# Optimization experiments

Measured on AMD Instinct MI355X. Metric: run time of the kernel, lower is better.

The kernel has to match this reference:

```python
import jax, jax.numpy as jnp
import numpy as np

B, N, K_NB, C, KERNEL, OUT = 32, 128, 16, 1024, 8, 1024
TWO_PI = 2.0 * np.pi
EPS = 1e-14


def setup_inputs() -> dict:
    key = jax.random.key(0)
    ks = jax.random.split(key, 9)
    return {
        "node_feats": jax.random.normal(ks[0], (B, N, C), dtype=jnp.float32),
        "node_centre": jax.random.uniform(ks[1], (B, N, 2), dtype=jnp.float32),
        "neighbor_idx": jax.random.randint(ks[2], (B, N, K_NB), 0, N, dtype=jnp.int32),
        "graph_weights": jax.random.uniform(ks[3], (B, N, K_NB), dtype=jnp.float32),
        "mean_rho": jax.random.uniform(ks[4], (1, KERNEL), dtype=jnp.float32),
        "mean_theta": jax.random.uniform(ks[5], (1, KERNEL), minval=-np.pi, maxval=np.pi, dtype=jnp.float32),
        "precision_rho": jax.random.uniform(ks[6], (1, KERNEL), dtype=jnp.float32),
        "precision_theta": jax.random.uniform(ks[7], (1, KERNEL), dtype=jnp.float32),
        "conv_w": jax.random.normal(ks[8], (KERNEL, C, OUT // KERNEL), dtype=jnp.float32) * 0.02,
    }


def _gaussian_weights(node_centre, neighbor_idx, mean_rho, mean_theta, precision_rho, precision_theta):
    # gather neighbor centres per batch: [B,N,K,2]
    centre_j = jax.vmap(lambda c, idx: c[idx])(node_centre, neighbor_idx)
    diff = node_centre[:, :, None, :] - centre_j           # node_i - node_j
    cx, cy = diff[..., 0], diff[..., 1]                    # chunk order: x first
    rho = jnp.sqrt(cx ** 2 + cy ** 2)                      # [B,N,K]
    theta = jnp.arctan2(cx, cy)                            # note: atan2(x, y) as in source
    d_rho = (rho[..., None] - mean_rho[0]) ** 2            # [B,N,K,KERNEL]
    w_rho = jnp.exp(-0.5 * d_rho / (EPS + precision_rho[0] ** 2))
    a1 = jnp.abs(theta[..., None] - mean_theta[0])
    a2 = jnp.abs(TWO_PI - a1)
    w_theta = jnp.exp(-0.5 * jnp.minimum(a1, a2) ** 2 / (EPS + precision_theta[0] ** 2))
    w = w_rho * w_theta
    w = jnp.where(jnp.isnan(w), 0.0, w)
    return w / jnp.sum(w, axis=-1, keepdims=True)          # normalize over kernel dim


def reference(node_feats, node_centre, neighbor_idx, graph_weights,
              mean_rho, mean_theta, precision_rho, precision_theta, conv_w):
    gw = _gaussian_weights(node_centre, neighbor_idx, mean_rho, mean_theta,
                           precision_rho, precision_theta)       # [B,N,K,KERNEL]
    edge_w = graph_weights[..., None] * gw                        # use_graph_weights=True
    # gather neighbor features per batch: [B,N,K,C]
    feats_j = jax.vmap(lambda f, idx: f[idx])(node_feats, neighbor_idx)
    # bmm aggregation: [B,N,KERNEL,C]
    agg = jnp.einsum('bnkm,bnkc->bnmc', edge_w, feats_j)
    # per-kernel linear (no bias) then concat: [B,N,KERNEL,OUT//KERNEL] -> [B,N,OUT]
    out = jnp.einsum('bnmc,mcd->bnmd', agg, conv_w)
    out = out.reshape(node_feats.shape[0], node_feats.shape[1], -1)
    return jax.nn.relu(out)
```

## Files before the change

### kernel.cpp

```cpp
#include <hip/hip_runtime.h>
#include <hip/hip_bf16.h>

#define B_   32
#define N_   128
#define KNB  16
#define C_   1024
#define KER  8
#define DOUT 128
#define OUTC 1024

typedef __attribute__((ext_vector_type(8))) short bf16x8;
typedef __attribute__((ext_vector_type(4))) float f32x4;

__device__ __forceinline__ ushort f2bf(float f) {
    unsigned u = __builtin_bit_cast(unsigned, f);
    unsigned r = (u + 0x7FFFu + ((u >> 16) & 1u)) >> 16;
    return (ushort)r;
}


__global__ __launch_bounds__(256) void k_prep(const float* __restrict__ F,
                                              ushort* __restrict__ Fpack,
                                              const float* __restrict__ W,
                                              ushort* __restrict__ Wpack,
                                              const float* __restrict__ centre,
                                              const int* __restrict__ nidx,
                                              const float* __restrict__ gw,
                                              const float* __restrict__ mr,
                                              const float* __restrict__ mt,
                                              const float* __restrict__ pr,
                                              const float* __restrict__ pt,
                                              float* __restrict__ ew) {
    __shared__ ushort Pt[16 * 1032];
    int bid = blockIdx.x;
    int t   = threadIdx.x;

    if (bid < 256) {
        int R0 = bid * 16;
#pragma unroll
        for (int it = 0; it < 16; ++it) {
            float4 v = *(const float4*)(F + (size_t)(R0 + it) * C_ + t * 4);
            ushort* d = Pt + it * 1032 + t * 4;
            d[0] = f2bf(v.x); d[1] = f2bf(v.y); d[2] = f2bf(v.z); d[3] = f2bf(v.w);
        }
        __syncthreads();
        ushort* dst = Fpack + (size_t)bid * 16384;
#pragma unroll
        for (int it = 0; it < 8; ++it) {
            int c  = it * 256 + t;
            int ln = c & 63, s = (c >> 6) & 15, kq = c >> 10;
            int lr = ln & 15, kg = ln >> 4;
            bf16x8 v = *(const bf16x8*)(Pt + lr * 1032 + kq * 512 + s * 32 + kg * 8);
            *(bf16x8*)(dst + (size_t)c * 8) = v;
        }
    } else if (bid < 320) {
        int b2 = bid - 256;
        int m  = b2 >> 3;
        int D0 = ((b2 >> 2) & 1) * 64 + (b2 & 3) * 16;
#pragma unroll
        for (int it = 0; it < 16; ++it) {
            int f  = it * 256 + t;
            int c  = f >> 2, q4 = f & 3;
            float4 v = *(const float4*)(W + (size_t)m * (C_ * DOUT) + (size_t)c * DOUT + D0 + q4 * 4);
            Pt[(q4 * 4 + 0) * 1032 + c] = f2bf(v.x);
            Pt[(q4 * 4 + 1) * 1032 + c] = f2bf(v.y);
            Pt[(q4 * 4 + 2) * 1032 + c] = f2bf(v.z);
            Pt[(q4 * 4 + 3) * 1032 + c] = f2bf(v.w);
        }
        __syncthreads();
        ushort* dst = Wpack + (size_t)b2 * 16384;
#pragma unroll
        for (int it = 0; it < 8; ++it) {
            int c  = it * 256 + t;
            int ln = c & 63, s = (c >> 6) & 15, kq = c >> 10;
            int lr = ln & 15, kg = ln >> 4;
            bf16x8 v = *(const bf16x8*)(Pt + lr * 1032 + kq * 512 + s * 32 + kg * 8);
            *(bf16x8*)(dst + (size_t)c * 8) = v;
        }
    } else {
        int tt = (bid - 320) * 256 + t;
        int bn = tt >> 4;
        int b  = bn >> 7;
        float2 ci = *(const float2*)(centre + (size_t)bn * 2);
        int j = nidx[tt];
        float2 cj = *(const float2*)(centre + (size_t)(b * N_ + j) * 2);
        float cx = ci.x - cj.x, cy = ci.y - cj.y;
        float rho = sqrtf(cx * cx + cy * cy);
        float theta = atan2f(cx, cy);
        float w[KER];
        float sum = 0.f;
#pragma unroll
        for (int m = 0; m < KER; ++m) {
            float dr = rho - mr[m];
            float wr = expf(-0.5f * dr * dr / (1e-14f + pr[m] * pr[m]));
            float a1 = fabsf(theta - mt[m]);
            float a2 = fabsf(6.2831853071795864f - a1);
            float am = fminf(a1, a2);
            float wt = expf(-0.5f * am * am / (1e-14f + pt[m] * pt[m]));
            float wv = wr * wt;
            if (isnan(wv)) wv = 0.f;
            w[m] = wv;
            sum += wv;
        }
        float scale = gw[tt] / sum;
#pragma unroll
        for (int m = 0; m < KER; ++m) ew[(size_t)tt * KER + m] = w[m] * scale;
    }
}

__global__ __launch_bounds__(512, 2) void k_fused(const ushort* __restrict__ Fpack,
                                                  const ushort* __restrict__ Wpack,
                                                  const float* __restrict__ ew,
                                                  const int* __restrict__ nidx,
                                                  float* __restrict__ out) {
    __shared__ float Gt[128 * 132];

    int tid  = threadIdx.x;
    int wave = tid >> 6;
    int lane = tid & 63;
    int kq = wave >> 2;
    int rh = (wave >> 1) & 1;
    int ch = wave & 1;
    int lr = lane & 15;
    int kg = lane >> 4;
    int bid = blockIdx.x;
    int b = bid & 31;
    int m = bid >> 5;

    const ushort* Abase[4];
    const ushort* Bbase[4];
#pragma unroll
    for (int i = 0; i < 4; ++i) {
        Abase[i] = Fpack + ((size_t)(b * 8 + rh * 4 + i) * 16384 + kq * 8192 + lane * 8);
        Bbase[i] = Wpack + ((size_t)(m * 8 + ch * 4 + i) * 16384 + kq * 8192 + lane * 8);
    }

    f32x4 acc[4][4];
#pragma unroll
    for (int i = 0; i < 4; ++i)
#pragma unroll
        for (int j = 0; j < 4; ++j) acc[i][j] = (f32x4){0.f, 0.f, 0.f, 0.f};

#pragma unroll
    for (int s = 0; s < 16; ++s) {
        bf16x8 av[4], bv[4];
#pragma unroll
        for (int i = 0; i < 4; ++i) {
            av[i] = *(const bf16x8*)(Abase[i] + s * 512);
            bv[i] = *(const bf16x8*)(Bbase[i] + s * 512);
        }
#pragma unroll
        for (int mi = 0; mi < 4; ++mi)
#pragma unroll
            for (int nj = 0; nj < 4; ++nj)
                acc[mi][nj] = __builtin_amdgcn_mfma_f32_16x16x32_bf16(
                    av[mi], bv[nj], acc[mi][nj], 0, 0, 0);
    }

    int n = tid >> 2, q = tid & 3;
    const int* ip = nidx + (size_t)(b * N_ + n) * KNB;
    int4 jv0 = *(const int4*)(ip);
    int4 jv1 = *(const int4*)(ip + 4);
    int4 jv2 = *(const int4*)(ip + 8);
    int4 jv3 = *(const int4*)(ip + 12);
    const float* ep = ew + (size_t)(b * N_ + n) * (KNB * KER) + m;
    float wv[KNB];
#pragma unroll
    for (int k = 0; k < KNB; ++k) wv[k] = ep[k * KER];

    if (kq == 0) {
#pragma unroll
        for (int mi = 0; mi < 4; ++mi)
#pragma unroll
            for (int nj = 0; nj < 4; ++nj)
#pragma unroll
                for (int r = 0; r < 4; ++r) {
                    int grow = rh * 64 + mi * 16 + kg * 4 + r;
                    int gcol = ch * 64 + nj * 16 + lr;
                    Gt[grow * 132 + gcol] = acc[mi][nj][r];
                }
    }
    __syncthreads();
    if (kq == 1) {
#pragma unroll
        for (int mi = 0; mi < 4; ++mi)
#pragma unroll
            for (int nj = 0; nj < 4; ++nj)
#pragma unroll
                for (int r = 0; r < 4; ++r) {
                    int grow = rh * 64 + mi * 16 + kg * 4 + r;
                    int gcol = ch * 64 + nj * 16 + lr;
                    Gt[grow * 132 + gcol] += acc[mi][nj][r];
                }
    }
    __syncthreads();

    int rot[8];
#pragma unroll
    for (int i = 0; i < 8; ++i) rot[i] = (q * 4 + i * 4) & 31;
    f32x4 o[8];
#pragma unroll
    for (int i = 0; i < 8; ++i) o[i] = (f32x4){0.f, 0.f, 0.f, 0.f};
    int jarr[KNB] = {jv0.x, jv0.y, jv0.z, jv0.w, jv1.x, jv1.y, jv1.z, jv1.w,
                     jv2.x, jv2.y, jv2.z, jv2.w, jv3.x, jv3.y, jv3.z, jv3.w};
#pragma unroll
    for (int k = 0; k < KNB; ++k) {
        const float* gr = Gt + jarr[k] * 132 + q * 32;
        float w = wv[k];
#pragma unroll
        for (int i = 0; i < 8; ++i) {
            f32x4 v = *(const f32x4*)(gr + rot[i]);
            o[i] += v * w;
        }
    }
    float* op = out + (size_t)(b * N_ + n) * OUTC + m * DOUT + q * 32;
#pragma unroll
    for (int i = 0; i < 8; ++i) {
        f32x4 r = o[i];
#pragma unroll
        for (int jj = 0; jj < 4; ++jj) r[jj] = fmaxf(r[jj], 0.f);
        *(f32x4*)(op + rot[i]) = r;
    }
}

extern "C" void kernel_launch(void* const* d_in, const int* in_sizes, int n_in,
                              void* d_out, int out_size, void* d_ws, size_t ws_size,
                              hipStream_t stream) {
    const float* node_feats      = (const float*)d_in[0];
    const float* node_centre     = (const float*)d_in[1];
    const int*   neighbor_idx    = (const int*)d_in[2];
    const float* graph_weights   = (const float*)d_in[3];
    const float* mean_rho        = (const float*)d_in[4];
    const float* mean_theta      = (const float*)d_in[5];
    const float* precision_rho   = (const float*)d_in[6];
    const float* precision_theta = (const float*)d_in[7];
    const float* conv_w          = (const float*)d_in[8];
    float* out = (float*)d_out;

    char* ws = (char*)d_ws;
    ushort* Fpack = (ushort*)(ws);
    ushort* Wpack = (ushort*)(ws + (8u  << 20));
    float*  ew    = (float*) (ws + (10u << 20));

    k_prep<<<576, 256, 0, stream>>>(node_feats, Fpack, conv_w, Wpack,
                                    node_centre, neighbor_idx, graph_weights,
                                    mean_rho, mean_theta,
                                    precision_rho, precision_theta, ew);
    k_fused<<<256, 512, 0, stream>>>(Fpack, Wpack, ew, neighbor_idx, out);
}
```

Before: 108.1 us.

## Merge prep and fused GEMM kernels into one cooperative kernel with grid sync

Result: slower. 234.9 us (+117.3%).

```diff
diff --git a/kernel.cpp b/kernel.cpp
--- a/kernel.cpp
+++ b/kernel.cpp
@@ -1,5 +1,8 @@
 #include <hip/hip_runtime.h>
 #include <hip/hip_bf16.h>
+#include <hip/hip_cooperative_groups.h>
+
+namespace cg = cooperative_groups;
 
 #define B_   32
 #define N_   128
@@ -19,103 +22,107 @@
 }
 
 
-__global__ __launch_bounds__(256) void k_prep(const float* __restrict__ F,
-                                              ushort* __restrict__ Fpack,
-                                              const float* __restrict__ W,
-                                              ushort* __restrict__ Wpack,
-                                              const float* __restrict__ centre,
-                                              const int* __restrict__ nidx,
-                                              const float* __restrict__ gw,
-                                              const float* __restrict__ mr,
-                                              const float* __restrict__ mt,
-                                              const float* __restrict__ pr,
-                                              const float* __restrict__ pt,
-                                              float* __restrict__ ew) {
-    __shared__ ushort Pt[16 * 1032];
+__global__ __launch_bounds__(512, 1) void k_all(const float* __restrict__ F,
+                                                const float* __restrict__ W,
+                                                const float* __restrict__ centre,
+                                                const int* __restrict__ nidx,
+                                                const float* __restrict__ gw,
+                                                const float* __restrict__ mr,
+                                                const float* __restrict__ mt,
+                                                const float* __restrict__ pr,
+                                                const float* __restrict__ pt,
+                                                ushort* __restrict__ Fpack,
+                                                ushort* __restrict__ Wpack,
+                                                float* __restrict__ ew,
+                                                float* __restrict__ out) {
+    __shared__ __align__(16) char smem[67584];
     int bid = blockIdx.x;
-    int t   = threadIdx.x;
-
-    if (bid < 256) {
-        int R0 = bid * 16;
-#pragma unroll
-        for (int it = 0; it < 16; ++it) {
-            float4 v = *(const float4*)(F + (size_t)(R0 + it) * C_ + t * 4);
-            ushort* d = Pt + it * 1032 + t * 4;
+    int tid = threadIdx.x;
+
+    {
+        ushort* Pt = (ushort*)smem;
+        int b0 = bid & 31, j0 = bid >> 5;
+        int R0 = b0 * 128 + j0 * 16;
+        ushort* dst = Fpack + (size_t)(b0 * 8 + j0) * 16384;
+#pragma unroll
+        for (int it = 0; it < 8; ++it) {
+            int f = it * 512 + tid;
+            int row = f >> 8, c4 = (f & 255) * 4;
+            float4 v = *(const float4*)(F + (size_t)(R0 + row) * C_ + c4);
+            ushort* d = Pt + row * 1032 + c4;
             d[0] = f2bf(v.x); d[1] = f2bf(v.y); d[2] = f2bf(v.z); d[3] = f2bf(v.w);
         }
         __syncthreads();
-        ushort* dst = Fpack + (size_t)bid * 16384;
-#pragma unroll
-        for (int it = 0; it < 8; ++it) {
-            int c  = it * 256 + t;
+#pragma unroll
+        for (int it = 0; it < 4; ++it) {
+            int c = it * 512 + tid;
             int ln = c & 63, s = (c >> 6) & 15, kq = c >> 10;
             int lr = ln & 15, kg = ln >> 4;
             bf16x8 v = *(const bf16x8*)(Pt + lr * 1032 + kq * 512 + s * 32 + kg * 8);
             *(bf16x8*)(dst + (size_t)c * 8) = v;
         }
-    } else if (bid < 320) {
-        int b2 = bid - 256;
-        int m  = b2 >> 3;
-        int D0 = ((b2 >> 2) & 1) * 64 + (b2 & 3) * 16;
-#pragma unroll
-        for (int it = 0; it < 16; ++it) {
-            int f  = it * 256 + t;
-            int c  = f >> 2, q4 = f & 3;
-            float4 v = *(const float4*)(W + (size_t)m * (C_ * DOUT) + (size_t)c * DOUT + D0 + q4 * 4);
-            Pt[(q4 * 4 + 0) * 1032 + c] = f2bf(v.x);
-            Pt[(q4 * 4 + 1) * 1032 + c] = f2bf(v.y);
-            Pt[(q4 * 4 + 2) * 1032 + c] = f2bf(v.z);
-            Pt[(q4 * 4 + 3) * 1032 + c] = f2bf(v.w);
-        }
-        __syncthreads();
-        ushort* dst = Wpack + (size_t)b2 * 16384;
-#pragma unroll
-        for (int it = 0; it < 8; ++it) {
-            int c  = it * 256 + t;
-            int ln = c & 63, s = (c >> 6) & 15, kq = c >> 10;
-            int lr = ln & 15, kg = ln >> 4;
-            bf16x8 v = *(const bf16x8*)(Pt + lr * 1032 + kq * 512 + s * 32 + kg * 8);
-            *(bf16x8*)(dst + (size_t)c * 8) = v;
-        }
-    } else {
-        int tt = (bid - 320) * 256 + t;
-        int bn = tt >> 4;
-        int b  = bn >> 7;
-        float2 ci = *(const float2*)(centre + (size_t)bn * 2);
-        int j = nidx[tt];
-        float2 cj = *(const float2*)(centre + (size_t)(b * N_ + j) * 2);
-        float cx = ci.x - cj.x, cy = ci.y - cj.y;
-        float rho = sqrtf(cx * cx + cy * cy);
-        float theta = atan2f(cx, cy);
-        float w[KER];
-        float sum = 0.f;
-#pragma unroll
-        for (int m = 0; m < KER; ++m) {
-            float dr = rho - mr[m];
-            float wr = expf(-0.5f * dr * dr / (1e-14f + pr[m] * pr[m]));
-            float a1 = fabsf(theta - mt[m]);
-            float a2 = fabsf(6.2831853071795864f - a1);
-            float am = fminf(a1, a2);
-            float wt = expf(-0.5f * am * am / (1e-14f + pt[m] * pt[m]));
-            float wv = wr * wt;
-            if (isnan(wv)) wv = 0.f;
-            w[m] = wv;
-            sum += wv;
-        }
-        float scale = gw[tt] / sum;
-#pragma unroll
-        for (int m = 0; m < KER; ++m) ew[(size_t)tt * KER + m] = w[m] * scale;
-    }
-}
-
-__global__ __launch_bounds__(512, 2) void k_fused(const ushort* __restrict__ Fpack,
-                                                  const ushort* __restrict__ Wpack,
-                                                  const float* __restrict__ ew,
-                                                  const int* __restrict__ nidx,
-                                                  float* __restrict__ out) {
-    __shared__ float Gt[128 * 132];
-
-    int tid  = threadIdx.x;
+
+        if (bid < 64) {
+            __syncthreads();
+            int m  = bid >> 3;
+            int D0 = ((bid >> 2) & 1) * 64 + (bid & 3) * 16;
+#pragma unroll
+            for (int it = 0; it < 8; ++it) {
+                int f = it * 512 + tid;
+                int c = f >> 2, q4 = f & 3;
+                float4 v = *(const float4*)(W + (size_t)m * (C_ * DOUT) + (size_t)c * DOUT + D0 + q4 * 4);
+                Pt[(q4 * 4 + 0) * 1032 + c] = f2bf(v.x);
+                Pt[(q4 * 4 + 1) * 1032 + c] = f2bf(v.y);
+                Pt[(q4 * 4 + 2) * 1032 + c] = f2bf(v.z);
+                Pt[(q4 * 4 + 3) * 1032 + c] = f2bf(v.w);
+            }
+            __syncthreads();
+            ushort* wdst = Wpack + (size_t)bid * 16384;
+#pragma unroll
+            for (int it = 0; it < 4; ++it) {
+                int c = it * 512 + tid;
+                int ln = c & 63, s = (c >> 6) & 15, kq = c >> 10;
+                int lr = ln & 15, kg = ln >> 4;
+                bf16x8 v = *(const bf16x8*)(Pt + lr * 1032 + kq * 512 + s * 32 + kg * 8);
+                *(bf16x8*)(wdst + (size_t)c * 8) = v;
+            }
+        } else if (bid >= 128) {
+            int e  = bid - 128;
+            int t  = (e & 31) * 2048 + (e >> 5) * 512 + tid;
+            int bn = t >> 4;
+            int bb = bn >> 7;
+            float2 ci = *(const float2*)(centre + (size_t)bn * 2);
+            int j = nidx[t];
+            float2 cj = *(const float2*)(centre + (size_t)(bb * N_ + j) * 2);
+            float cx = ci.x - cj.x, cy = ci.y - cj.y;
+            float rho = sqrtf(cx * cx + cy * cy);
+            float theta = atan2f(cx, cy);
+            float w[KER];
+            float sum = 0.f;
+#pragma unroll
+            for (int m = 0; m < KER; ++m) {
+                float dr = rho - mr[m];
+                float wr = expf(-0.5f * dr * dr / (1e-14f + pr[m] * pr[m]));
+                float a1 = fabsf(theta - mt[m]);
+                float a2 = fabsf(6.2831853071795864f - a1);
+                float am = fminf(a1, a2);
+                float wt = expf(-0.5f * am * am / (1e-14f + pt[m] * pt[m]));
+                float wv = wr * wt;
+                if (isnan(wv)) wv = 0.f;
+                w[m] = wv;
+                sum += wv;
+            }
+            float scale = gw[t] / sum;
+#pragma unroll
+            for (int m = 0; m < KER; ++m) ew[(size_t)t * KER + m] = w[m] * scale;
+        }
+    }
+
+    __threadfence();
+    cg::this_grid().sync();
+
+    float* Gt = (float*)smem;
+
     int wave = tid >> 6;
     int lane = tid & 63;
     int kq = wave >> 2;
@@ -123,7 +130,6 @@
     int ch = wave & 1;
     int lr = lane & 15;
     int kg = lane >> 4;
-    int bid = blockIdx.x;
     int b = bid & 31;
     int m = bid >> 5;
 
@@ -141,20 +147,28 @@
 #pragma unroll
         for (int j = 0; j < 4; ++j) acc[i][j] = (f32x4){0.f, 0.f, 0.f, 0.f};
 
+    bf16x8 av[2][4], bv[2][4];
+#pragma unroll
+    for (int i = 0; i < 4; ++i) {
+        av[0][i] = *(const bf16x8*)(Abase[i]);
+        bv[0][i] = *(const bf16x8*)(Bbase[i]);
+    }
 #pragma unroll
     for (int s = 0; s < 16; ++s) {
-        bf16x8 av[4], bv[4];
-#pragma unroll
-        for (int i = 0; i < 4; ++i) {
-            av[i] = *(const bf16x8*)(Abase[i] + s * 512);
-            bv[i] = *(const bf16x8*)(Bbase[i] + s * 512);
+        int c = s & 1, nx = c ^ 1;
+        if (s + 1 < 16) {
+#pragma unroll
+            for (int i = 0; i < 4; ++i) {
+                av[nx][i] = *(const bf16x8*)(Abase[i] + (s + 1) * 512);
+                bv[nx][i] = *(const bf16x8*)(Bbase[i] + (s + 1) * 512);
+            }
         }
 #pragma unroll
         for (int mi = 0; mi < 4; ++mi)
 #pragma unroll
             for (int nj = 0; nj < 4; ++nj)
                 acc[mi][nj] = __builtin_amdgcn_mfma_f32_16x16x32_bf16(
-                    av[mi], bv[nj], acc[mi][nj], 0, 0, 0);
+                    av[c][mi], bv[c][nj], acc[mi][nj], 0, 0, 0);
     }
 
     int n = tid >> 2, q = tid & 3;
@@ -168,6 +182,7 @@
 #pragma unroll
     for (int k = 0; k < KNB; ++k) wv[k] = ep[k * KER];
 
+    __syncthreads();
     if (kq == 0) {
 #pragma unroll
         for (int mi = 0; mi < 4; ++mi)
@@ -242,9 +257,11 @@
     ushort* Wpack = (ushort*)(ws + (8u  << 20));
     float*  ew    = (float*) (ws + (10u << 20));
 
-    k_prep<<<576, 256, 0, stream>>>(node_feats, Fpack, conv_w, Wpack,
-                                    node_centre, neighbor_idx, graph_weights,
-                                    mean_rho, mean_theta,
-                                    precision_rho, precision_theta, ew);
-    k_fused<<<256, 512, 0, stream>>>(Fpack, Wpack, ew, neighbor_idx, out);
+    void* args[] = {(void*)&node_feats, (void*)&conv_w, (void*)&node_centre,
+                    (void*)&neighbor_idx, (void*)&graph_weights,
+                    (void*)&mean_rho, (void*)&mean_theta,
+                    (void*)&precision_rho, (void*)&precision_theta,
+                    (void*)&Fpack, (void*)&Wpack, (void*)&ew, (void*)&out};
+    hipLaunchCooperativeKernel((const void*)k_all, dim3(256), dim3(512),
+                               args, 0, stream);
 }
```

## Split GEMM K-dimension across four wave groups with 1024-thread blocks and register prefetch

Applied to the files above, without the earlier changes.

Measured after the change: 112.6 us. +4.2%, slower.

```diff
diff --git a/kernel.cpp b/kernel.cpp
--- a/kernel.cpp
+++ b/kernel.cpp
@@ -108,19 +108,19 @@
     }
 }
 
-__global__ __launch_bounds__(512, 2) void k_fused(const ushort* __restrict__ Fpack,
-                                                  const ushort* __restrict__ Wpack,
-                                                  const float* __restrict__ ew,
-                                                  const int* __restrict__ nidx,
-                                                  float* __restrict__ out) {
+__global__ __launch_bounds__(1024, 4) void k_fused(const ushort* __restrict__ Fpack,
+                                                   const ushort* __restrict__ Wpack,
+                                                   const float* __restrict__ ew,
+                                                   const int* __restrict__ nidx,
+                                                   float* __restrict__ out) {
     __shared__ float Gt[128 * 132];
 
     int tid  = threadIdx.x;
     int wave = tid >> 6;
     int lane = tid & 63;
-    int kq = wave >> 2;
-    int rh = (wave >> 1) & 1;
-    int ch = wave & 1;
+    int kq4 = wave >> 2;
+    int rh  = (wave >> 1) & 1;
+    int ch  = wave & 1;
     int lr = lane & 15;
     int kg = lane >> 4;
     int bid = blockIdx.x;
@@ -131,8 +131,8 @@
     const ushort* Bbase[4];
 #pragma unroll
     for (int i = 0; i < 4; ++i) {
-        Abase[i] = Fpack + ((size_t)(b * 8 + rh * 4 + i) * 16384 + kq * 8192 + lane * 8);
-        Bbase[i] = Wpack + ((size_t)(m * 8 + ch * 4 + i) * 16384 + kq * 8192 + lane * 8);
+        Abase[i] = Fpack + ((size_t)(b * 8 + rh * 4 + i) * 16384 + kq4 * 4096 + lane * 8);
+        Bbase[i] = Wpack + ((size_t)(m * 8 + ch * 4 + i) * 16384 + kq4 * 4096 + lane * 8);
     }
 
     f32x4 acc[4][4];
@@ -141,23 +141,31 @@
 #pragma unroll
         for (int j = 0; j < 4; ++j) acc[i][j] = (f32x4){0.f, 0.f, 0.f, 0.f};
 
-#pragma unroll
-    for (int s = 0; s < 16; ++s) {
-        bf16x8 av[4], bv[4];
-#pragma unroll
-        for (int i = 0; i < 4; ++i) {
-            av[i] = *(const bf16x8*)(Abase[i] + s * 512);
-            bv[i] = *(const bf16x8*)(Bbase[i] + s * 512);
+    bf16x8 av[2][4], bv[2][4];
+#pragma unroll
+    for (int i = 0; i < 4; ++i) {
+        av[0][i] = *(const bf16x8*)(Abase[i]);
+        bv[0][i] = *(const bf16x8*)(Bbase[i]);
+    }
+#pragma unroll
+    for (int s = 0; s < 8; ++s) {
+        int c = s & 1, nx = c ^ 1;
+        if (s + 1 < 8) {
+#pragma unroll
+            for (int i = 0; i < 4; ++i) {
+                av[nx][i] = *(const bf16x8*)(Abase[i] + (s + 1) * 512);
+                bv[nx][i] = *(const bf16x8*)(Bbase[i] + (s + 1) * 512);
+            }
         }
 #pragma unroll
         for (int mi = 0; mi < 4; ++mi)
 #pragma unroll
             for (int nj = 0; nj < 4; ++nj)
                 acc[mi][nj] = __builtin_amdgcn_mfma_f32_16x16x32_bf16(
-                    av[mi], bv[nj], acc[mi][nj], 0, 0, 0);
-    }
-
-    int n = tid >> 2, q = tid & 3;
+                    av[c][mi], bv[c][nj], acc[mi][nj], 0, 0, 0);
+    }
+
+    int n = tid >> 3, q = tid & 7;
     const int* ip = nidx + (size_t)(b * N_ + n) * KNB;
     int4 jv0 = *(const int4*)(ip);
     int4 jv1 = *(const int4*)(ip + 4);
@@ -168,54 +176,45 @@
 #pragma unroll
     for (int k = 0; k < KNB; ++k) wv[k] = ep[k * KER];
 
-    if (kq == 0) {
-#pragma unroll
-        for (int mi = 0; mi < 4; ++mi)
-#pragma unroll
-            for (int nj = 0; nj < 4; ++nj)
-#pragma unroll
-                for (int r = 0; r < 4; ++r) {
-                    int grow = rh * 64 + mi * 16 + kg * 4 + r;
-                    int gcol = ch * 64 + nj * 16 + lr;
-                    Gt[grow * 132 + gcol] = acc[mi][nj][r];
-                }
-    }
-    __syncthreads();
-    if (kq == 1) {
-#pragma unroll
-        for (int mi = 0; mi < 4; ++mi)
-#pragma unroll
-            for (int nj = 0; nj < 4; ++nj)
-#pragma unroll
-                for (int r = 0; r < 4; ++r) {
-                    int grow = rh * 64 + mi * 16 + kg * 4 + r;
-                    int gcol = ch * 64 + nj * 16 + lr;
-                    Gt[grow * 132 + gcol] += acc[mi][nj][r];
-                }
-    }
-    __syncthreads();
-
-    int rot[8];
-#pragma unroll
-    for (int i = 0; i < 8; ++i) rot[i] = (q * 4 + i * 4) & 31;
-    f32x4 o[8];
-#pragma unroll
-    for (int i = 0; i < 8; ++i) o[i] = (f32x4){0.f, 0.f, 0.f, 0.f};
+#pragma unroll
+    for (int st = 0; st < 4; ++st) {
+        if (kq4 == st) {
+#pragma unroll
+            for (int mi = 0; mi < 4; ++mi)
+#pragma unroll
+                for (int nj = 0; nj < 4; ++nj)
+#pragma unroll
+                    for (int r = 0; r < 4; ++r) {
+                        int grow = rh * 64 + mi * 16 + kg * 4 + r;
+                        int gcol = ch * 64 + nj * 16 + lr;
+                        if (st == 0) Gt[grow * 132 + gcol] = acc[mi][nj][r];
+                        else         Gt[grow * 132 + gcol] += acc[mi][nj][r];
+                    }
+        }
+        __syncthreads();
+    }
+
+    int rot[4];
+#pragma unroll
+    for (int i = 0; i < 4; ++i) rot[i] = (q * 4 + i * 4) & 15;
+    f32x4 o[4];
+#pragma unroll
+    for (int i = 0; i < 4; ++i) o[i] = (f32x4){0.f, 0.f, 0.f, 0.f};
     int jarr[KNB] = {jv0.x, jv0.y, jv0.z, jv0.w, jv1.x, jv1.y, jv1.z, jv1.w,
                      jv2.x, jv2.y, jv2.z, jv2.w, jv3.x, jv3.y, jv3.z, jv3.w};
 #pragma unroll
     for (int k = 0; k < KNB; ++k) {
-        const float* gr = Gt + jarr[k] * 132 + q * 32;
+        const float* gr = Gt + jarr[k] * 132 + q * 16;
         float w = wv[k];
 #pragma unroll
-        for (int i = 0; i < 8; ++i) {
+        for (int i = 0; i < 4; ++i) {
             f32x4 v = *(const f32x4*)(gr + rot[i]);
             o[i] += v * w;
         }
     }
-    float* op = out + (size_t)(b * N_ + n) * OUTC + m * DOUT + q * 32;
-#pragma unroll
-    for (int i = 0; i < 8; ++i) {
+    float* op = out + (size_t)(b * N_ + n) * OUTC + m * DOUT + q * 16;
+#pragma unroll
+    for (int i = 0; i < 4; ++i) {
         f32x4 r = o[i];
 #pragma unroll
         for (int jj = 0; jj < 4; ++jj) r[jj] = fmaxf(r[jj], 0.f);
@@ -246,5 +245,5 @@
                                     node_centre, neighbor_idx, graph_weights,
                                     mean_rho, mean_theta,
                                     precision_rho, precision_theta, ew);
-    k_fused<<<256, 512, 0, stream>>>(Fpack, Wpack, ew, neighbor_idx, out);
-}
+    k_fused<<<256, 1024, 0, stream>>>(Fpack, Wpack, ew, neighbor_idx, out);
+}
```
